# Kernel optimization log

Measured on AMD Instinct MI355X. Metric: run time of the kernel, lower is better.

Reference implementation:

```python
import jax, jax.numpy as jnp
import numpy as np

KS = 3          # deform kernel size
N = KS * KS     # 9 sampling taps per pixel
PAD = 1         # zero padding applied before sampling (nn.ZeroPad2d)
BN_EPS = 1e-5


def conv2d(x, w, b=None, stride=1, padding=0):
    out = jax.lax.conv_general_dilated(
        x, w, (stride, stride), [(padding, padding)] * 2,
        dimension_numbers=('NCHW', 'OIHW', 'NCHW'))
    if b is not None:
        out = out + b[None, :, None, None]
    return out


def setup_inputs() -> dict:
    key = jax.random.key(0)
    ks = jax.random.split(key, 6)
    inC, outC = 128, 256
    B, H, W = 8, 64, 64

    def kaiming(k, shape):
        fan_in = shape[1] * shape[2] * shape[3]
        return jax.random.normal(k, shape, jnp.float32) / np.float32(np.sqrt(fan_in))

    return {
        'x': jax.random.normal(ks[0], (B, inC, H, W), jnp.float32),
        'w_offset': kaiming(ks[1], (2 * N, inC, 3, 3)) * 0.1,  # small offsets, realistic
        'b_offset': jnp.zeros((2 * N,), jnp.float32),
        'w_mask': kaiming(ks[2], (N, inC, 3, 3)),
        'b_mask': jnp.zeros((N,), jnp.float32),
        'w_conv': kaiming(ks[3], (outC, inC, KS, KS)),
        'bn_gamma': jnp.ones((outC,), jnp.float32),
        'bn_beta': jnp.zeros((outC,), jnp.float32),
        'bn_mean': jax.random.normal(ks[4], (outC,), jnp.float32) * 0.1,
        'bn_var': jnp.ones((outC,), jnp.float32) + jax.random.uniform(ks[5], (outC,), jnp.float32) * 0.1,
    }


def deform_conv(x, w_offset, b_offset, w_mask, b_mask, w_conv):
    B, C, H, W = x.shape
    dt = x.dtype

    offset = conv2d(x, w_offset, b_offset, 1, 1)               # (B, 2N, H, W)
    m = jax.nn.sigmoid(conv2d(x, w_mask, b_mask, 1, 1))        # (B, N, H, W)

    # kernel grid offsets p_n (first N channels = rows, last N = cols)
    rng = jnp.arange(-(KS - 1) // 2, (KS - 1) // 2 + 1, dtype=dt)
    pnx, pny = jnp.meshgrid(rng, rng, indexing='ij')
    p_n = jnp.concatenate([pnx.reshape(-1), pny.reshape(-1)])[None, :, None, None]

    # base positions p_0 (torch impl starts at 1, sampling on padded input)
    p0x = jnp.broadcast_to(jnp.arange(1, H + 1, dtype=dt)[:, None], (H, W))
    p0y = jnp.broadcast_to(jnp.arange(1, W + 1, dtype=dt)[None, :], (H, W))
    p_0 = jnp.concatenate([jnp.tile(p0x[None], (N, 1, 1)),
                           jnp.tile(p0y[None], (N, 1, 1))])[None]  # (1, 2N, H, W)

    p = (offset + p_n + p_0).transpose(0, 2, 3, 1)             # (B, H, W, 2N)

    xp = jnp.pad(x, ((0, 0), (0, 0), (PAD, PAD), (PAD, PAD)))
    Hp, Wp = H + 2 * PAD, W + 2 * PAD

    px, py = p[..., :N], p[..., N:]
    fx, fy = jnp.floor(px), jnp.floor(py)
    q_lt_x = jnp.clip(fx, 0, Hp - 1)
    q_lt_y = jnp.clip(fy, 0, Wp - 1)
    q_rb_x = jnp.clip(fx + 1, 0, Hp - 1)
    q_rb_y = jnp.clip(fy + 1, 0, Wp - 1)
    px = jnp.clip(px, 0, Hp - 1)
    py = jnp.clip(py, 0, Wp - 1)

    # bilinear weights (faithful to the reference torch formulas)
    g_lt = (1 + (q_lt_x - px)) * (1 + (q_lt_y - py))
    g_rb = (1 - (q_rb_x - px)) * (1 - (q_rb_y - py))
    g_lb = (1 + (q_lt_x - px)) * (1 - (q_rb_y - py))
    g_rt = (1 - (q_rb_x - px)) * (1 + (q_lt_y - py))

    xp_flat = xp.reshape(B, C, Hp * Wp)

    def gather(qx, qy):
        idx = (qx.astype(jnp.int32) * Wp + qy.astype(jnp.int32)).reshape(B, 1, -1)
        out = jnp.take_along_axis(xp_flat,
                                  jnp.broadcast_to(idx, (B, C, idx.shape[-1])), axis=2)
        return out.reshape(B, C, H, W, N)

    x_off = (g_lt[:, None] * gather(q_lt_x, q_lt_y)
             + g_rb[:, None] * gather(q_rb_x, q_rb_y)
             + g_lb[:, None] * gather(q_lt_x, q_rb_y)
             + g_rt[:, None] * gather(q_rb_x, q_lt_y))       # (B, C, H, W, N)

    x_off = x_off * m.transpose(0, 2, 3, 1)[:, None]          # modulation

    # (B,C,H,W,ks,ks) -> (B,C,H*ks,W*ks)  (equivalent to _reshape_x_offset)
    x_off = x_off.reshape(B, C, H, W, KS, KS).transpose(0, 1, 2, 4, 3, 5)
    x_off = x_off.reshape(B, C, H * KS, W * KS)

    return conv2d(x_off, w_conv, None, KS, 0)                 # (B, outC, H, W)


def reference(x, w_offset, b_offset, w_mask, b_mask, w_conv,
              bn_gamma, bn_beta, bn_mean, bn_var):
    y = deform_conv(x, w_offset, b_offset, w_mask, b_mask, w_conv)
    inv = jax.lax.rsqrt(bn_var + BN_EPS)
    scale = (bn_gamma * inv)[None, :, None, None]
    shift = (bn_beta - bn_mean * bn_gamma * inv)[None, :, None, None]
    return jax.nn.relu(y * scale + shift)
```

## Files before the change

kernel.cpp:

```cpp
#include <hip/hip_runtime.h>
#include <math.h>

#define BB 8
#define CC 128
#define HH 64
#define WW 64
#define NPTS 9
#define OUTC 256
#define HW (HH*WW)
#define KTOT (CC*NPTS)
#define BK 288
#define AP 290
#define WROWS 6

typedef __attribute__((ext_vector_type(8))) short bf16x8;
typedef __attribute__((ext_vector_type(4))) float f32x4;

__device__ unsigned short g_wT[OUTC * KTOT];
__device__ unsigned short g_woT[32 * KTOT];

__device__ __forceinline__ unsigned short f2bf(float f) {
    unsigned int u = __builtin_bit_cast(unsigned int, f);
    unsigned int r = (u + 0x7FFFu + ((u >> 16) & 1u)) >> 16;
    return (unsigned short)r;
}

__device__ __forceinline__ unsigned cvtpk(float lo, float hi) {
    unsigned r;
    asm("v_cvt_pk_bf16_f32 %0, %1, %2" : "=v"(r) : "v"(lo), "v"(hi));
    return r;
}
__device__ __forceinline__ float bflo(unsigned w) { return __builtin_bit_cast(float, w << 16); }
__device__ __forceinline__ float bfhi(unsigned w) { return __builtin_bit_cast(float, w & 0xFFFF0000u); }

__device__ __forceinline__ int orig_k(int k) {
    int cb = k / BK, r = k % BK;
    int pair = r / 18, r2 = r % 18;
    int n = r2 >> 1, half = r2 & 1;
    return (cb * 32 + pair * 2 + half) * NPTS + n;
}

__global__ __launch_bounds__(256) void prep_kernel(
    const float* __restrict__ wo, const float* __restrict__ wm,
    const float* __restrict__ wc)
{
    int idx = blockIdx.x * 256 + threadIdx.x;
    const int T1 = 32 * KTOT;
    if (idx < T1) {
        int nn = idx / KTOT, k = idx - nn * KTOT;
        int ok = orig_k(k);
        float v = (nn < 18) ? wo[nn * KTOT + ok]
                            : (nn < 27 ? wm[(nn - 18) * KTOT + ok] : 0.f);
        g_woT[idx] = f2bf(v);
    } else if (idx < T1 + OUTC * KTOT) {
        int j = idx - T1;
        int oc = j / KTOT, k = j - oc * KTOT;
        g_wT[j] = f2bf(wc[oc * KTOT + orig_k(k)]);
    }
}

struct PF { uint2 w[WROWS]; };

__device__ __forceinline__ void issue(PF& pf, const float* __restrict__ xb,
                                      int h, int g, int tid) {
    if (g >= 8) return;
    int cb = g & 3;
    int q = tid >> 6, col = tid & 63;
    const float* base = xb + (size_t)(cb * 32 + 4 * q) * HW + col;
    #pragma unroll
    for (int r = 0; r < WROWS; ++r) {
        int gr = h - 2 + r;
        bool v = (gr >= 0) & (gr < HH);
        float a0 = v ? base[0 * HW + gr * WW] : 0.f;
        float a1 = v ? base[1 * HW + gr * WW] : 0.f;
        float a2 = v ? base[2 * HW + gr * WW] : 0.f;
        float a3 = v ? base[3 * HW + gr * WW] : 0.f;
        pf.w[r].x = cvtpk(a0, a1);
        pf.w[r].y = cvtpk(a2, a3);
    }
}

__device__ __forceinline__ void commit(uint2* win, const PF& pf, int tid) {
    uint2* wp = win + (tid >> 6) * 384 + (tid & 63);
    #pragma unroll
    for (int r = 0; r < WROWS; ++r) wp[r * 64] = pf.w[r];
}

__global__ __launch_bounds__(512) __attribute__((amdgpu_waves_per_eu(4, 4)))
void fused_kernel(
    const float* __restrict__ x,
    const float* __restrict__ b_offset, const float* __restrict__ b_mask,
    const float* __restrict__ bn_gamma, const float* __restrict__ bn_beta,
    const float* __restrict__ bn_mean,  const float* __restrict__ bn_var,
    float* __restrict__ out)
{
    __shared__ unsigned short Atile[64][AP];
    __shared__ uint2 win[8 * 384];
    __shared__ float4 gtab[NPTS][64];
    __shared__ uint2  otab[NPTS][64];
    float* ovf = (float*)win;

    int bid = blockIdx.x;
    int blk = (bid & 7) * 64 + (bid >> 3);
    int b = blk >> 6, h = blk & 63;
    int tid  = threadIdx.x;
    int lane = tid & 63;
    int wv   = __builtin_amdgcn_readfirstlane(tid >> 6);
    int l15  = lane & 15;
    int kg   = lane >> 4;
    int spix = lane;

    const float* xb = x + (size_t)b * CC * HW;
    unsigned* AtU = (unsigned*)&Atile[0][0];

    int mi_a = wv & 3, nf_a = wv >> 2;
    f32x4 s1acc = {0.f, 0.f, 0.f, 0.f};

    PF pf; issue(pf, xb, h, 0, tid);
    for (int cb = 0; cb < 4; ++cb) {
        commit(win, pf, tid);
        {
            const uint2* base = win + wv * 384;
            #pragma unroll
            for (int tap = 0; tap < 9; ++tap) {
                int ky = tap / 3, kx = tap % 3;
                int col  = spix + kx - 1;
                int colc = min(max(col, 0), WW - 1);
                uint2 v = base[(ky + 1) * 64 + colc];
                bool cv = (col >= 0) & (col < WW);
                AtU[spix * 145 + (2 * wv) * 9 + tap]     = cv ? v.x : 0u;
                AtU[spix * 145 + (2 * wv + 1) * 9 + tap] = cv ? v.y : 0u;
            }
        }
        issue(pf, xb, h, cb + 1, tid);
        __syncthreads();
        __builtin_amdgcn_s_setprio(1);
        for (int q = 0; q < 9; ++q) {
            int koff = q * 32 + kg * 8;
            bf16x8 af = *(const bf16x8*)&Atile[mi_a * 16 + l15][koff];
            int nn = nf_a * 16 + l15;
            bf16x8 bfr = *(const bf16x8*)&g_woT[nn * KTOT + cb * BK + koff];
            s1acc = __builtin_amdgcn_mfma_f32_16x16x32_bf16(af, bfr, s1acc, 0, 0, 0);
        }
        __builtin_amdgcn_s_setprio(0);
        __syncthreads();
    }

    #pragma unroll
    for (int j = 0; j < 4; ++j) {
        float val = s1acc[j];
        int nn   = nf_a * 16 + l15;
        int pixl = mi_a * 16 + kg * 4 + j;
        if (nn < 9) {
            ovf[nn * 64 + pixl] = val + b_offset[nn] + (float)(nn / 3 - 1) + (float)(h + 1);
        } else if (nn < 18) {
            int n = nn - 9;
            ovf[576 + n * 64 + pixl] = val + b_offset[nn] + (float)(n % 3 - 1) + (float)(pixl + 1);
        } else if (nn < 27) {
            int n = nn - 18;
            float sg = val + b_mask[n];
            ovf[1152 + n * 64 + pixl] = 1.f / (1.f + expf(-sg));
        }
    }
    __syncthreads();

    if (tid < 64) {
        int t = tid;
        #pragma unroll
        for (int n = 0; n < NPTS; ++n) {
            float px = ovf[n * 64 + t];
            float py = ovf[576 + n * 64 + t];
            float m  = ovf[1152 + n * 64 + t];
            float fx = floorf(px), fy = floorf(py);
            float qltx = fminf(fmaxf(fx,       0.f), 65.f);
            float qlty = fminf(fmaxf(fy,       0.f), 65.f);
            float qrbx = fminf(fmaxf(fx + 1.f, 0.f), 65.f);
            float qrby = fminf(fmaxf(fy + 1.f, 0.f), 65.f);
            float pxc  = fminf(fmaxf(px, 0.f), 65.f);
            float pyc  = fminf(fmaxf(py, 0.f), 65.f);
            float glt = (1.f + (qltx - pxc)) * (1.f + (qlty - pyc)) * m;
            float grb = (1.f - (qrbx - pxc)) * (1.f - (qrby - pyc)) * m;
            float glb = (1.f + (qltx - pxc)) * (1.f - (qrby - pyc)) * m;
            float grt = (1.f - (qrbx - pxc)) * (1.f + (qlty - pyc)) * m;
            int i0 = (int)qltx - 1, j0 = (int)qlty - 1;
            int i1 = (int)qrbx - 1, j1 = (int)qrby - 1;
            bool v00 = (i0 >= 0) & (i0 < HH) & (j0 >= 0) & (j0 < WW);
            bool v11 = (i1 >= 0) & (i1 < HH) & (j1 >= 0) & (j1 < WW);
            bool v01 = (i0 >= 0) & (i0 < HH) & (j1 >= 0) & (j1 < WW);
            bool v10 = (i1 >= 0) & (i1 < HH) & (j0 >= 0) & (j0 < WW);
            float4 g;
            g.x = v00 ? glt : 0.f;
            g.y = v11 ? grb : 0.f;
            g.z = v01 ? glb : 0.f;
            g.w = v10 ? grt : 0.f;
            gtab[n][t] = g;
            bool okr0 = ((i0 >= h - 2) & (i0 <= h + 3)) | !(v00 | v01);
            bool okr1 = ((i1 >= h - 2) & (i1 <= h + 3)) | !(v11 | v10);
            bool ok = okr0 & okr1;
            int r0w = min(max(i0 - (h - 2), 0), WROWS - 1);
            int r1w = min(max(i1 - (h - 2), 0), WROWS - 1);
            int r0g = min(max(i0, 0), HH - 1);
            int r1g = min(max(i1, 0), HH - 1);
            int j0c = min(max(j0, 0), WW - 1);
            int j1c = min(max(j1, 0), WW - 1);
            int o  = ok ? (r0w * WW + j0c) : (r0g * WW + j0c);
            int dr = ok ? (r1w - r0w) : (r1g - r0g);
            int dj = j1c - j0c;
            unsigned o00 = (unsigned)o;
            unsigned o11 = (unsigned)(o + dr * WW + dj);
            unsigned o01 = (unsigned)(o + dj);
            unsigned o10 = (unsigned)(o + dr * WW);
            uint2 ot;
            ot.x = (o00 | (ok ? 0u : 0x8000u)) | (o11 << 16);
            ot.y = o01 | (o10 << 16);
            otab[n][t] = ot;
        }
    }
    __syncthreads();

    f32x4 acc[4][2];
    #pragma unroll
    for (int mi = 0; mi < 4; ++mi)
        #pragma unroll
        for (int ni = 0; ni < 2; ++ni)
            acc[mi][ni] = (f32x4){0.f, 0.f, 0.f, 0.f};

    int oc0 = wv * 32;

    for (int cb = 0; cb < 4; ++cb) {
        commit(win, pf, tid);
        {
            const uint2* baseq = win + wv * 384;
            const float* xg = xb + (size_t)(cb * 32 + 4 * wv) * HW;
            #pragma unroll
            for (int n = 0; n < NPTS; ++n) {
                float4 g  = gtab[n][spix];
                uint2  ot = otab[n][spix];
                int o00 = ot.x & 0x7FFF;
                int o11 = ot.x >> 16;
                int o01 = ot.y & 0xFFFF;
                int o10 = ot.y >> 16;
                float v0, v1, v2, v3;
                if (!(ot.x & 0x8000u)) {
                    uint2 c00 = baseq[o00];
                    uint2 c11 = baseq[o11];
                    uint2 c01 = baseq[o01];
                    uint2 c10 = baseq[o10];
                    v0 =       g.x * bflo(c00.x);
                    v0 = fmaf(g.y, bflo(c11.x), v0);
                    v0 = fmaf(g.z, bflo(c01.x), v0);
                    v0 = fmaf(g.w, bflo(c10.x), v0);
                    v1 =       g.x * bfhi(c00.x);
                    v1 = fmaf(g.y, bfhi(c11.x), v1);
                    v1 = fmaf(g.z, bfhi(c01.x), v1);
                    v1 = fmaf(g.w, bfhi(c10.x), v1);
                    v2 =       g.x * bflo(c00.y);
                    v2 = fmaf(g.y, bflo(c11.y), v2);
                    v2 = fmaf(g.z, bflo(c01.y), v2);
                    v2 = fmaf(g.w, bflo(c10.y), v2);
                    v3 =       g.x * bfhi(c00.y);
                    v3 = fmaf(g.y, bfhi(c11.y), v3);
                    v3 = fmaf(g.z, bfhi(c01.y), v3);
                    v3 = fmaf(g.w, bfhi(c10.y), v3);
                } else {
                    const float* x0 = xg;
                    const float* x1 = xg + HW;
                    const float* x2 = xg + 2 * HW;
                    const float* x3 = xg + 3 * HW;
                    v0 = g.x*x0[o00]; v0 = fmaf(g.y, x0[o11], v0); v0 = fmaf(g.z, x0[o01], v0); v0 = fmaf(g.w, x0[o10], v0);
                    v1 = g.x*x1[o00]; v1 = fmaf(g.y, x1[o11], v1); v1 = fmaf(g.z, x1[o01], v1); v1 = fmaf(g.w, x1[o10], v1);
                    v2 = g.x*x2[o00]; v2 = fmaf(g.y, x2[o11], v2); v2 = fmaf(g.z, x2[o01], v2); v2 = fmaf(g.w, x2[o10], v2);
                    v3 = g.x*x3[o00]; v3 = fmaf(g.y, x3[o11], v3); v3 = fmaf(g.z, x3[o01], v3); v3 = fmaf(g.w, x3[o10], v3);
                }
                AtU[spix * 145 + (2 * wv) * 9 + n]     = cvtpk(v0, v1);
                AtU[spix * 145 + (2 * wv + 1) * 9 + n] = cvtpk(v2, v3);
            }
        }
        issue(pf, xb, h, 5 + cb, tid);
        __syncthreads();
        __builtin_amdgcn_s_setprio(1);
        for (int q = 0; q < 9; ++q) {
            int koff = q * 32 + kg * 8;
            bf16x8 af[4];
            #pragma unroll
            for (int mi = 0; mi < 4; ++mi)
                af[mi] = *(const bf16x8*)&Atile[mi * 16 + l15][koff];
            #pragma unroll
            for (int ni = 0; ni < 2; ++ni) {
                int oc = oc0 + ni * 16 + l15;
                bf16x8 bfr = *(const bf16x8*)&g_wT[oc * KTOT + cb * BK + koff];
                #pragma unroll
                for (int mi = 0; mi < 4; ++mi)
                    acc[mi][ni] = __builtin_amdgcn_mfma_f32_16x16x32_bf16(af[mi], bfr, acc[mi][ni], 0, 0, 0);
            }
        }
        __builtin_amdgcn_s_setprio(0);
        __syncthreads();
    }

    #pragma unroll
    for (int ni = 0; ni < 2; ++ni) {
        int oc = oc0 + ni * 16 + l15;
        float inv   = 1.f / sqrtf(bn_var[oc] + 1e-5f);
        float scale = bn_gamma[oc] * inv;
        float shift = bn_beta[oc] - bn_mean[oc] * scale;
        float* op = out + ((size_t)b * OUTC + oc) * HW + h * WW + kg * 4;
        #pragma unroll
        for (int mi = 0; mi < 4; ++mi) {
            f32x4 o4;
            #pragma unroll
            for (int j = 0; j < 4; ++j) {
                float v = fmaf(acc[mi][ni][j], scale, shift);
                o4[j] = v > 0.f ? v : 0.f;
            }
            *(f32x4*)(op + mi * 16) = o4;
        }
    }
}

extern "C" void kernel_launch(void* const* d_in, const int* in_sizes, int n_in,
                              void* d_out, int out_size, void* d_ws, size_t ws_size,
                              hipStream_t stream) {
    (void)in_sizes; (void)n_in; (void)out_size; (void)d_ws; (void)ws_size;
    const float* x        = (const float*)d_in[0];
    const float* w_offset = (const float*)d_in[1];
    const float* b_offset = (const float*)d_in[2];
    const float* w_mask   = (const float*)d_in[3];
    const float* b_mask   = (const float*)d_in[4];
    const float* w_conv   = (const float*)d_in[5];
    const float* bn_gamma = (const float*)d_in[6];
    const float* bn_beta  = (const float*)d_in[7];
    const float* bn_mean  = (const float*)d_in[8];
    const float* bn_var   = (const float*)d_in[9];
    float* out = (float*)d_out;

    int prep_elems = 32 * KTOT + OUTC * KTOT;
    prep_kernel<<<(prep_elems + 255) / 256, 256, 0, stream>>>(w_offset, w_mask, w_conv);
    fused_kernel<<<BB * HH, 512, 0, stream>>>(x, b_offset, b_mask,
                                              bn_gamma, bn_beta, bn_mean, bn_var, out);
}
```

Before: 85.22 us.

## Split offset conv into separate K-split kernel and halve output channels per block

Moves the offset/mask convolution into its own kernel that splits the input channels in two and writes partial sums to a global buffer, which the main kernel adds up before computing the bilinear tables. The main kernel now covers 128 output channels per block (1024 blocks instead of 512), and works in 16-channel chunks with K padded to 160. The aim is more blocks and higher occupancy so the GPU is better filled. The cost is an extra launch, a global round trip for the partials, the offset/bilinear setup being recomputed by both channel-half blocks, and wasted MFMA work on the zero-padded K.

```diff
diff --git a/kernel.cpp b/kernel.cpp
--- a/kernel.cpp
+++ b/kernel.cpp
@@ -9,22 +9,24 @@
 #define OUTC 256
 #define HW (HH*WW)
 #define KTOT (CC*NPTS)
-#define BK 288
-#define AP 290
+#define NCHUNK 8
+#define BKP 160
+#define KP (NCHUNK*BKP)
+#define APW 81
 #define WROWS 6
 
 typedef __attribute__((ext_vector_type(8))) short bf16x8;
 typedef __attribute__((ext_vector_type(4))) float f32x4;
 
-__device__ unsigned short g_wT[OUTC * KTOT];
-__device__ unsigned short g_woT[32 * KTOT];
+__device__ unsigned short g_wT[OUTC * KP];
+__device__ unsigned short g_woT[32 * KP];
+__device__ float g_part[512 * 2 * 27 * 64];
 
 __device__ __forceinline__ unsigned short f2bf(float f) {
     unsigned int u = __builtin_bit_cast(unsigned int, f);
     unsigned int r = (u + 0x7FFFu + ((u >> 16) & 1u)) >> 16;
     return (unsigned short)r;
 }
-
 __device__ __forceinline__ unsigned cvtpk(float lo, float hi) {
     unsigned r;
     asm("v_cvt_pk_bf16_f32 %0, %1, %2" : "=v"(r) : "v"(lo), "v"(hi));
@@ -34,10 +36,11 @@
 __device__ __forceinline__ float bfhi(unsigned w) { return __builtin_bit_cast(float, w & 0xFFFF0000u); }
 
 __device__ __forceinline__ int orig_k(int k) {
-    int cb = k / BK, r = k % BK;
+    int chunk = k / BKP, r = k % BKP;
+    if (r >= 144) return -1;
     int pair = r / 18, r2 = r % 18;
     int n = r2 >> 1, half = r2 & 1;
-    return (cb * 32 + pair * 2 + half) * NPTS + n;
+    return (chunk * 16 + pair * 2 + half) * NPTS + n;
 }
 
 __global__ __launch_bounds__(256) void prep_kernel(
@@ -45,132 +48,150 @@
     const float* __restrict__ wc)
 {
     int idx = blockIdx.x * 256 + threadIdx.x;
-    const int T1 = 32 * KTOT;
+    const int T1 = 32 * KP;
     if (idx < T1) {
-        int nn = idx / KTOT, k = idx - nn * KTOT;
+        int nn = idx / KP, k = idx - nn * KP;
         int ok = orig_k(k);
-        float v = (nn < 18) ? wo[nn * KTOT + ok]
-                            : (nn < 27 ? wm[(nn - 18) * KTOT + ok] : 0.f);
+        float v = 0.f;
+        if (ok >= 0) {
+            if (nn < 18)      v = wo[nn * KTOT + ok];
+            else if (nn < 27) v = wm[(nn - 18) * KTOT + ok];
+        }
         g_woT[idx] = f2bf(v);
-    } else if (idx < T1 + OUTC * KTOT) {
+    } else if (idx < T1 + OUTC * KP) {
         int j = idx - T1;
-        int oc = j / KTOT, k = j - oc * KTOT;
-        g_wT[j] = f2bf(wc[oc * KTOT + orig_k(k)]);
-    }
-}
-
-struct PF { uint2 w[WROWS]; };
+        int oc = j / KP, k = j - oc * KP;
+        int ok = orig_k(k);
+        g_wT[j] = f2bf(ok >= 0 ? wc[oc * KTOT + ok] : 0.f);
+    }
+}
+
+struct PF { unsigned w[WROWS]; };
 
 __device__ __forceinline__ void issue(PF& pf, const float* __restrict__ xb,
-                                      int h, int g, int tid) {
-    if (g >= 8) return;
-    int cb = g & 3;
-    int q = tid >> 6, col = tid & 63;
-    const float* base = xb + (size_t)(cb * 32 + 4 * q) * HW + col;
+                                      int h, int chunk, int wv, int lane) {
+    const float* base = xb + (size_t)(chunk * 16 + 2 * wv) * HW + lane;
     #pragma unroll
     for (int r = 0; r < WROWS; ++r) {
         int gr = h - 2 + r;
         bool v = (gr >= 0) & (gr < HH);
-        float a0 = v ? base[0 * HW + gr * WW] : 0.f;
-        float a1 = v ? base[1 * HW + gr * WW] : 0.f;
-        float a2 = v ? base[2 * HW + gr * WW] : 0.f;
-        float a3 = v ? base[3 * HW + gr * WW] : 0.f;
-        pf.w[r].x = cvtpk(a0, a1);
-        pf.w[r].y = cvtpk(a2, a3);
-    }
-}
-
-__device__ __forceinline__ void commit(uint2* win, const PF& pf, int tid) {
-    uint2* wp = win + (tid >> 6) * 384 + (tid & 63);
+        float a0 = v ? base[gr * WW] : 0.f;
+        float a1 = v ? base[HW + gr * WW] : 0.f;
+        pf.w[r] = cvtpk(a0, a1);
+    }
+}
+__device__ __forceinline__ void commit(unsigned* win, const PF& pf, int wv, int lane) {
+    unsigned* wp = win + wv * 384 + lane;
     #pragma unroll
     for (int r = 0; r < WROWS; ++r) wp[r * 64] = pf.w[r];
 }
 
-__global__ __launch_bounds__(512) __attribute__((amdgpu_waves_per_eu(4, 4)))
-void fused_kernel(
+__global__ __launch_bounds__(512) __attribute__((amdgpu_waves_per_eu(8, 8)))
+void offconv_kernel(const float* __restrict__ x)
+{
+    __shared__ unsigned short Atile[64][2 * APW];
+    __shared__ unsigned win[8 * 384];
+
+    int bid = blockIdx.x;
+    int b = bid & 7;
+    int local = bid >> 3;
+    int h = local >> 1, kh = local & 1;
+    int tid  = threadIdx.x;
+    int lane = tid & 63;
+    int wv   = __builtin_amdgcn_readfirstlane(tid >> 6);
+    int l15  = lane & 15;
+    int kg   = lane >> 4;
+
+    const float* xb = x + (size_t)b * CC * HW;
+    unsigned* AtU = (unsigned*)&Atile[0][0];
+
+    AtU[(tid & 63) * APW + 72 + (tid >> 6)] = 0u;
+
+    int mi_a = wv & 3, nf_a = wv >> 2;
+    f32x4 s1acc = {0.f, 0.f, 0.f, 0.f};
+
+    PF pf; issue(pf, xb, h, kh * 4, wv, lane);
+    for (int i = 0; i < 4; ++i) {
+        int c = kh * 4 + i;
+        commit(win, pf, wv, lane);
+        {
+            const unsigned* basep = win + wv * 384;
+            #pragma unroll
+            for (int tap = 0; tap < 9; ++tap) {
+                int ky = tap / 3, kx = tap % 3;
+                int col  = lane + kx - 1;
+                int colc = min(max(col, 0), WW - 1);
+                unsigned w = basep[(ky + 1) * 64 + colc];
+                w = (col >= 0 && col < WW) ? w : 0u;
+                AtU[lane * APW + wv * 9 + tap] = w;
+            }
+        }
+        if (i < 3) issue(pf, xb, h, c + 1, wv, lane);
+        __syncthreads();
+        __builtin_amdgcn_s_setprio(1);
+        for (int q = 0; q < 5; ++q) {
+            int koff = q * 32 + kg * 8;
+            bf16x8 af = *(const bf16x8*)&Atile[mi_a * 16 + l15][koff];
+            int nn = nf_a * 16 + l15;
+            bf16x8 bfr = *(const bf16x8*)&g_woT[nn * KP + c * BKP + koff];
+            s1acc = __builtin_amdgcn_mfma_f32_16x16x32_bf16(af, bfr, s1acc, 0, 0, 0);
+        }
+        __builtin_amdgcn_s_setprio(0);
+        __syncthreads();
+    }
+
+    int blk = b * 64 + h;
+    int nn = nf_a * 16 + l15;
+    if (nn < 27) {
+        #pragma unroll
+        for (int j = 0; j < 4; ++j) {
+            int pixl = mi_a * 16 + kg * 4 + j;
+            g_part[((size_t)(blk * 2 + kh) * 27 + nn) * 64 + pixl] = s1acc[j];
+        }
+    }
+}
+
+__global__ __launch_bounds__(512) __attribute__((amdgpu_waves_per_eu(4, 8)))
+void main_kernel(
     const float* __restrict__ x,
     const float* __restrict__ b_offset, const float* __restrict__ b_mask,
     const float* __restrict__ bn_gamma, const float* __restrict__ bn_beta,
     const float* __restrict__ bn_mean,  const float* __restrict__ bn_var,
     float* __restrict__ out)
 {
-    __shared__ unsigned short Atile[64][AP];
-    __shared__ uint2 win[8 * 384];
+    __shared__ unsigned short Atile[64][2 * APW];
+    __shared__ unsigned win[8 * 384];
     __shared__ float4 gtab[NPTS][64];
     __shared__ uint2  otab[NPTS][64];
-    float* ovf = (float*)win;
 
     int bid = blockIdx.x;
-    int blk = (bid & 7) * 64 + (bid >> 3);
-    int b = blk >> 6, h = blk & 63;
+    int b = bid & 7;
+    int local = bid >> 3;
+    int h = local >> 1, oct = local & 1;
     int tid  = threadIdx.x;
     int lane = tid & 63;
     int wv   = __builtin_amdgcn_readfirstlane(tid >> 6);
     int l15  = lane & 15;
     int kg   = lane >> 4;
-    int spix = lane;
 
     const float* xb = x + (size_t)b * CC * HW;
     unsigned* AtU = (unsigned*)&Atile[0][0];
-
-    int mi_a = wv & 3, nf_a = wv >> 2;
-    f32x4 s1acc = {0.f, 0.f, 0.f, 0.f};
-
-    PF pf; issue(pf, xb, h, 0, tid);
-    for (int cb = 0; cb < 4; ++cb) {
-        commit(win, pf, tid);
-        {
-            const uint2* base = win + wv * 384;
-            #pragma unroll
-            for (int tap = 0; tap < 9; ++tap) {
-                int ky = tap / 3, kx = tap % 3;
-                int col  = spix + kx - 1;
-                int colc = min(max(col, 0), WW - 1);
-                uint2 v = base[(ky + 1) * 64 + colc];
-                bool cv = (col >= 0) & (col < WW);
-                AtU[spix * 145 + (2 * wv) * 9 + tap]     = cv ? v.x : 0u;
-                AtU[spix * 145 + (2 * wv + 1) * 9 + tap] = cv ? v.y : 0u;
-            }
-        }
-        issue(pf, xb, h, cb + 1, tid);
-        __syncthreads();
-        __builtin_amdgcn_s_setprio(1);
-        for (int q = 0; q < 9; ++q) {
-            int koff = q * 32 + kg * 8;
-            bf16x8 af = *(const bf16x8*)&Atile[mi_a * 16 + l15][koff];
-            int nn = nf_a * 16 + l15;
-            bf16x8 bfr = *(const bf16x8*)&g_woT[nn * KTOT + cb * BK + koff];
-            s1acc = __builtin_amdgcn_mfma_f32_16x16x32_bf16(af, bfr, s1acc, 0, 0, 0);
-        }
-        __builtin_amdgcn_s_setprio(0);
-        __syncthreads();
-    }
-
-    #pragma unroll
-    for (int j = 0; j < 4; ++j) {
-        float val = s1acc[j];
-        int nn   = nf_a * 16 + l15;
-        int pixl = mi_a * 16 + kg * 4 + j;
-        if (nn < 9) {
-            ovf[nn * 64 + pixl] = val + b_offset[nn] + (float)(nn / 3 - 1) + (float)(h + 1);
-        } else if (nn < 18) {
-            int n = nn - 9;
-            ovf[576 + n * 64 + pixl] = val + b_offset[nn] + (float)(n % 3 - 1) + (float)(pixl + 1);
-        } else if (nn < 27) {
-            int n = nn - 18;
-            float sg = val + b_mask[n];
-            ovf[1152 + n * 64 + pixl] = 1.f / (1.f + expf(-sg));
-        }
-    }
-    __syncthreads();
+    int blk = b * 64 + h;
+
+    AtU[(tid & 63) * APW + 72 + (tid >> 6)] = 0u;
 
     if (tid < 64) {
         int t = tid;
+        const float* p0 = &g_part[(size_t)(blk * 2 + 0) * 27 * 64];
+        const float* p1 = &g_part[(size_t)(blk * 2 + 1) * 27 * 64];
         #pragma unroll
         for (int n = 0; n < NPTS; ++n) {
-            float px = ovf[n * 64 + t];
-            float py = ovf[576 + n * 64 + t];
-            float m  = ovf[1152 + n * 64 + t];
+            float px = p0[n * 64 + t] + p1[n * 64 + t]
+                     + b_offset[n] + (float)(n / 3 - 1) + (float)(h + 1);
+            float py = p0[(9 + n) * 64 + t] + p1[(9 + n) * 64 + t]
+                     + b_offset[9 + n] + (float)(n % 3 - 1) + (float)(t + 1);
+            float sg = p0[(18 + n) * 64 + t] + p1[(18 + n) * 64 + t] + b_mask[n];
+            float m  = 1.f / (1.f + expf(-sg));
             float fx = floorf(px), fy = floorf(py);
             float qltx = fminf(fmaxf(fx,       0.f), 65.f);
             float qlty = fminf(fmaxf(fy,       0.f), 65.f);
@@ -218,89 +239,74 @@
     }
     __syncthreads();
 
-    f32x4 acc[4][2];
+    f32x4 acc[4];
     #pragma unroll
-    for (int mi = 0; mi < 4; ++mi)
-        #pragma unroll
-        for (int ni = 0; ni < 2; ++ni)
-            acc[mi][ni] = (f32x4){0.f, 0.f, 0.f, 0.f};
-
-    int oc0 = wv * 32;
-
-    for (int cb = 0; cb < 4; ++cb) {
-        commit(win, pf, tid);
+    for (int mi = 0; mi < 4; ++mi) acc[mi] = (f32x4){0.f, 0.f, 0.f, 0.f};
+    int oc0 = oct * 128 + wv * 16;
+
+    PF pf; issue(pf, xb, h, 0, wv, lane);
+    for (int c = 0; c < NCHUNK; ++c) {
+        commit(win, pf, wv, lane);
         {
-            const uint2* baseq = win + wv * 384;
-            const float* xg = xb + (size_t)(cb * 32 + 4 * wv) * HW;
+            const unsigned* basep = win + wv * 384;
+            const float* xgA = xb + (size_t)(c * 16 + 2 * wv) * HW;
+            const float* xgB = xgA + HW;
             #pragma unroll
             for (int n = 0; n < NPTS; ++n) {
-                float4 g  = gtab[n][spix];
-                uint2  ot = otab[n][spix];
+                float4 g  = gtab[n][lane];
+                uint2  ot = otab[n][lane];
                 int o00 = ot.x & 0x7FFF;
                 int o11 = ot.x >> 16;
                 int o01 = ot.y & 0xFFFF;
                 int o10 = ot.y >> 16;
-                float v0, v1, v2, v3;
+                float v0, v1;
                 if (!(ot.x & 0x8000u)) {
-                    uint2 c00 = baseq[o00];
-                    uint2 c11 = baseq[o11];
-                    uint2 c01 = baseq[o01];
-                    uint2 c10 = baseq[o10];
-                    v0 =       g.x * bflo(c00.x);
-                    v0 = fmaf(g.y, bflo(c11.x), v0);
-                    v0 = fmaf(g.z, bflo(c01.x), v0);
-                    v0 = fmaf(g.w, bflo(c10.x), v0);
-                    v1 =       g.x * bfhi(c00.x);
-                    v1 = fmaf(g.y, bfhi(c11.x), v1);
-                    v1 = fmaf(g.z, bfhi(c01.x), v1);
-                    v1 = fmaf(g.w, bfhi(c10.x), v1);
-                    v2 =       g.x * bflo(c00.y);
-                    v2 = fmaf(g.y, bflo(c11.y), v2);
-                    v2 = fmaf(g.z, bflo(c01.y), v2);
-                    v2 = fmaf(g.w, bflo(c10.y), v2);
-                    v3 =       g.x * bfhi(c00.y);
-                    v3 = fmaf(g.y, bfhi(c11.y), v3);
-                    v3 = fmaf(g.z, bfhi(c01.y), v3);
-                    v3 = fmaf(g.w, bfhi(c10.y), v3);
+                    unsigned w00 = basep[o00];
+                    unsigned w11 = basep[o11];
+                    unsigned w01 = basep[o01];
+                    unsigned w10 = basep[o10];
+                    v0 =       g.x * bflo(w00);
+                    v0 = fmaf(g.y, bflo(w11), v0);
+                    v0 = fmaf(g.z, bflo(w01), v0);
+                    v0 = fmaf(g.w, bflo(w10), v0);
+                    v1 =       g.x * bfhi(w00);
+                    v1 = fmaf(g.y, bfhi(w11), v1);
+                    v1 = fmaf(g.z, bfhi(w01), v1);
+                    v1 = fmaf(g.w, bfhi(w10), v1);
                 } else {
-                    const float* x0 = xg;
-                    const float* x1 = xg + HW;
-                    const float* x2 = xg + 2 * HW;
-                    const float* x3 = xg + 3 * HW;
-                    v0 = g.x*x0[o00]; v0 = fmaf(g.y, x0[o11], v0); v0 = fmaf(g.z, x0[o01], v0); v0 = fmaf(g.w, x0[o10], v0);
-                    v1 = g.x*x1[o00]; v1 = fmaf(g.y, x1[o11], v1); v1 = fmaf(g.z, x1[o01], v1); v1 = fmaf(g.w, x1[o10], v1);
-                    v2 = g.x*x2[o00]; v2 = fmaf(g.y, x2[o11], v2); v2 = fmaf(g.z, x2[o01], v2); v2 = fmaf(g.w, x2[o10], v2);
-                    v3 = g.x*x3[o00]; v3 = fmaf(g.y, x3[o11], v3); v3 = fmaf(g.z, x3[o01], v3); v3 = fmaf(g.w, x3[o10], v3);
+                    v0 =       g.x * xgA[o00];
+                    v0 = fmaf(g.y, xgA[o11], v0);
+                    v0 = fmaf(g.z, xgA[o01], v0);
+                    v0 = fmaf(g.w, xgA[o10], v0);
+                    v1 =       g.x * xgB[o00];
+                    v1 = fmaf(g.y, xgB[o11], v1);
+                    v1 = fmaf(g.z, xgB[o01], v1);
+                    v1 = fmaf(g.w, xgB[o10], v1);
                 }
-                AtU[spix * 145 + (2 * wv) * 9 + n]     = cvtpk(v0, v1);
-                AtU[spix * 145 + (2 * wv + 1) * 9 + n] = cvtpk(v2, v3);
+                AtU[lane * APW + wv * 9 + n] = cvtpk(v0, v1);
             }
         }
-        issue(pf, xb, h, 5 + cb, tid);
+        if (c < NCHUNK - 1) issue(pf, xb, h, c + 1, wv, lane);
         __syncthreads();
         __builtin_amdgcn_s_setprio(1);
-        for (int q = 0; q < 9; ++q) {
+        for (int q = 0; q < 5; ++q) {
             int koff = q * 32 + kg * 8;
             bf16x8 af[4];
             #pragma unroll
             for (int mi = 0; mi < 4; ++mi)
                 af[mi] = *(const bf16x8*)&Atile[mi * 16 + l15][koff];
-            #pragma unroll
-            for (int ni = 0; ni < 2; ++ni) {
-                int oc = oc0 + ni * 16 + l15;
-                bf16x8 bfr = *(const bf16x8*)&g_wT[oc * KTOT + cb * BK + koff];
-                #pragma unroll
-                for (int mi = 0; mi < 4; ++mi)
-                    acc[mi][ni] = __builtin_amdgcn_mfma_f32_16x16x32_bf16(af[mi], bfr, acc[mi][ni], 0, 0, 0);
-            }
+            int oc = oc0 + l15;
+            bf16x8 bfr = *(const bf16x8*)&g_wT[(size_t)oc * KP + c * BKP + koff];
+            #pragma unroll
+            for (int mi = 0; mi < 4; ++mi)
+                acc[mi] = __builtin_amdgcn_mfma_f32_16x16x32_bf16(af[mi], bfr, acc[mi], 0, 0, 0);
         }
         __builtin_amdgcn_s_setprio(0);
         __syncthreads();
     }
 
-    #pragma unroll
-    for (int ni = 0; ni < 2; ++ni) {
-        int oc = oc0 + ni * 16 + l15;
+    {
+        int oc = oc0 + l15;
         float inv   = 1.f / sqrtf(bn_var[oc] + 1e-5f);
         float scale = bn_gamma[oc] * inv;
         float shift = bn_beta[oc] - bn_mean[oc] * scale;
@@ -310,7 +316,7 @@
             f32x4 o4;
             #pragma unroll
             for (int j = 0; j < 4; ++j) {
-                float v = fmaf(acc[mi][ni][j], scale, shift);
+                float v = fmaf(acc[mi][j], scale, shift);
                 o4[j] = v > 0.f ? v : 0.f;
             }
             *(f32x4*)(op + mi * 16) = o4;
@@ -334,8 +340,9 @@
     const float* bn_var   = (const float*)d_in[9];
     float* out = (float*)d_out;
 
-    int prep_elems = 32 * KTOT + OUTC * KTOT;
+    int prep_elems = 32 * KP + OUTC * KP;
     prep_kernel<<<(prep_elems + 255) / 256, 256, 0, stream>>>(w_offset, w_mask, w_conv);
-    fused_kernel<<<BB * HH, 512, 0, stream>>>(x, b_offset, b_mask,
-                                              bn_gamma, bn_beta, bn_mean, bn_var, out);
-}
+    offconv_kernel<<<1024, 512, 0, stream>>>(x);
+    main_kernel<<<1024, 512, 0, stream>>>(x, b_offset, b_mask,
+                                          bn_gamma, bn_beta, bn_mean, bn_var, out);
+}
```

New measurement: 127.9 us. 50.1% more time.
